# Kernel tuning notes

Measured on AMD Instinct MI355X. Metric: run time of the kernel, lower is better.

The kernel has to match this reference:

```python
import jax, jax.numpy as jnp
import numpy as np

MSK_TOK_ID = 4
SPC_TOK_IDS = (0, 1, 2, 3)
REG_W, MSK_W, SPC_W = 1.0, 1.0, 0.01
B, S, V = 8, 1024, 32000


def setup_inputs() -> dict:
    key = jax.random.key(0)
    k1, k2, k3 = jax.random.split(key, 3)
    logits_pred = jax.random.normal(k1, (B, S, V), dtype=jnp.float32)
    tokens_inp = jax.random.randint(k2, (B, S), 0, 100, dtype=jnp.int32)
    tokens_tgt = jax.random.randint(k3, (B, S), 0, V, dtype=jnp.int32)
    return {"logits_pred": logits_pred, "tokens_inp": tokens_inp, "tokens_tgt": tokens_tgt}


def _loss(logits_pred, tokens_inp, tokens_tgt):
    # torch: softmax then log(gather) == log_softmax then gather (more stable, same math)
    logp = jax.nn.log_softmax(logits_pred, axis=-1)                 # [B,S,V]
    nll = -jnp.take_along_axis(logp, tokens_tgt[..., None].astype(jnp.int32), axis=2)[..., 0]  # [B,S]

    mask_msk = tokens_inp == MSK_TOK_ID
    mask_spc = jnp.zeros_like(mask_msk)
    for t in SPC_TOK_IDS:
        mask_spc = mask_spc | (tokens_inp == t)
    mask_reg = (~mask_msk) & (~mask_spc)

    def cat_mean(mask):
        cnt = jnp.sum(mask, axis=1)                                  # [B]
        s = jnp.sum(jnp.where(mask, nll, 0.0), axis=1)               # [B]
        present = cnt > 0
        mean = jnp.where(present, s / jnp.maximum(cnt, 1).astype(nll.dtype), 0.0)
        return mean, present.astype(nll.dtype)

    m_reg, p_reg = cat_mean(mask_reg)
    m_msk, p_msk = cat_mean(mask_msk)
    m_spc, p_spc = cat_mean(mask_spc)

    num = m_reg * REG_W * p_reg + m_msk * MSK_W * p_msk + m_spc * SPC_W * p_spc
    tw = p_reg * REG_W + p_msk * MSK_W + p_spc * SPC_W              # per-item total_weight
    loss = jnp.mean(num / tw)

    def cat_avg(mean, present):
        n = jnp.sum(present)
        return jnp.where(n > 0, jnp.sum(mean) / jnp.maximum(n, 1.0), 0.0)

    return loss, cat_avg(m_reg, p_reg), cat_avg(m_msk, p_msk), cat_avg(m_spc, p_spc)


def reference(logits_pred, tokens_inp, tokens_tgt):
    # returns (loss, reg_toks_loss, msk_toks_loss, spc_toks_loss)
    return _loss(logits_pred, tokens_inp, tokens_tgt)
```

## Files before the change

### kernel.cpp

```cpp
#include <hip/hip_runtime.h>
#include <math.h>

#define NB 8
#define NS 1024
#define NV 32000

__global__ __launch_bounds__(256)
void nll_kernel(const float* __restrict__ logits,
                const int* __restrict__ tgt,
                float* __restrict__ nll) {
    const int row = blockIdx.x;
    const float* rp = logits + (size_t)row * NV;
    const int tid = threadIdx.x;

    float m = -INFINITY, s = 0.0f;
    const float4* rp4 = (const float4*)rp;
    const int n4 = NV / 4;
    for (int i = tid; i < n4; i += 256) {
        float4 x = rp4[i];
        float m4 = fmaxf(fmaxf(x.x, x.y), fmaxf(x.z, x.w));
        float nm = fmaxf(m, m4);
        s = s * __expf(m - nm)
          + __expf(x.x - nm) + __expf(x.y - nm)
          + __expf(x.z - nm) + __expf(x.w - nm);
        m = nm;
    }

    #pragma unroll
    for (int off = 1; off < 64; off <<= 1) {
        float om = __shfl_xor(m, off, 64);
        float os = __shfl_xor(s, off, 64);
        float nm = fmaxf(m, om);
        s = s * __expf(m - nm) + os * __expf(om - nm);
        m = nm;
    }

    __shared__ float sm[4], ss[4];
    const int wave = tid >> 6, lane = tid & 63;
    if (lane == 0) { sm[wave] = m; ss[wave] = s; }
    __syncthreads();
    if (tid == 0) {
        float M = sm[0], Sv = ss[0];
        #pragma unroll
        for (int w = 1; w < 4; ++w) {
            float om = sm[w], os = ss[w];
            float nm = fmaxf(M, om);
            Sv = Sv * __expf(M - nm) + os * __expf(om - nm);
            M = nm;
        }
        float lse = __logf(Sv) + M;
        float lt = rp[tgt[row]];
        nll[row] = lse - lt;
    }
}

__global__ __launch_bounds__(256)
void batch_reduce_kernel(const int* __restrict__ inp,
                         const float* __restrict__ nll,
                         float* __restrict__ part) {
    const int b = blockIdx.x;
    const int tid = threadIdx.x;
    float acc[6] = {0.f, 0.f, 0.f, 0.f, 0.f, 0.f};
    for (int i = tid; i < NS; i += 256) {
        int tok = inp[b * NS + i];
        float v = nll[b * NS + i];
        if (tok == 4)                 { acc[2] += v; acc[3] += 1.f; }
        else if ((unsigned)tok < 4u)  { acc[4] += v; acc[5] += 1.f; }
        else                          { acc[0] += v; acc[1] += 1.f; }
    }
    __shared__ float buf[6][256];
    #pragma unroll
    for (int k = 0; k < 6; ++k) buf[k][tid] = acc[k];
    __syncthreads();
    for (int off = 128; off > 0; off >>= 1) {
        if (tid < off) {
            #pragma unroll
            for (int k = 0; k < 6; ++k) buf[k][tid] += buf[k][tid + off];
        }
        __syncthreads();
    }
    if (tid == 0) {
        #pragma unroll
        for (int k = 0; k < 6; ++k) part[b * 6 + k] = buf[k][0];
    }
}

__global__ void finalize_kernel(const float* __restrict__ part,
                                float* __restrict__ out) {
    if (threadIdx.x != 0 || blockIdx.x != 0) return;
    const float W[3] = {1.0f, 1.0f, 0.01f};
    float loss_acc = 0.f;
    float sum_m[3] = {0.f, 0.f, 0.f};
    float sum_p[3] = {0.f, 0.f, 0.f};
    for (int b = 0; b < NB; ++b) {
        float num = 0.f, tw = 0.f;
        #pragma unroll
        for (int k = 0; k < 3; ++k) {
            float s = part[b * 6 + 2 * k];
            float c = part[b * 6 + 2 * k + 1];
            float p = (c > 0.f) ? 1.f : 0.f;
            float mean = (c > 0.f) ? (s / c) : 0.f;
            num += mean * W[k] * p;
            tw  += p * W[k];
            sum_m[k] += mean;
            sum_p[k] += p;
        }
        loss_acc += num / tw;
    }
    out[0] = loss_acc / (float)NB;
    #pragma unroll
    for (int k = 0; k < 3; ++k)
        out[1 + k] = (sum_p[k] > 0.f) ? (sum_m[k] / fmaxf(sum_p[k], 1.f)) : 0.f;
}

extern "C" void kernel_launch(void* const* d_in, const int* in_sizes, int n_in,
                              void* d_out, int out_size, void* d_ws, size_t ws_size,
                              hipStream_t stream) {
    const float* logits = (const float*)d_in[0];
    const int*   inp    = (const int*)d_in[1];
    const int*   tgt    = (const int*)d_in[2];
    float* out = (float*)d_out;
    float* nll  = (float*)d_ws;
    float* part = nll + NB * NS;

    nll_kernel<<<NB * NS, 256, 0, stream>>>(logits, tgt, nll);
    batch_reduce_kernel<<<NB, 256, 0, stream>>>(inp, nll, part);
    finalize_kernel<<<1, 64, 0, stream>>>(part, out);
}
```

Measured before the change: 188.7 us.

## Use unshifted exp-sum fast path for logsumexp and fuse reduce with finalize

The row kernel now sums exp(x) directly without a running max, dropping the per-element rescale exponentials. It falls back to a two-pass max-then-sum only when the sum underflows or overflows. The batch reduction and finalize kernels are merged into one 512-thread block with one wave per batch using shuffle reductions, which removes a launch. The unshifted sum can lose precision for large-magnitude logits but stays correct for well-scaled inputs.

```diff
diff --git a/kernel.cpp b/kernel.cpp
--- a/kernel.cpp
+++ b/kernel.cpp
@@ -12,105 +12,130 @@
     const int row = blockIdx.x;
     const float* rp = logits + (size_t)row * NV;
     const int tid = threadIdx.x;
-
-    float m = -INFINITY, s = 0.0f;
     const float4* rp4 = (const float4*)rp;
     const int n4 = NV / 4;
+
+    float s0 = 0.f, s1 = 0.f;
     for (int i = tid; i < n4; i += 256) {
         float4 x = rp4[i];
-        float m4 = fmaxf(fmaxf(x.x, x.y), fmaxf(x.z, x.w));
-        float nm = fmaxf(m, m4);
-        s = s * __expf(m - nm)
-          + __expf(x.x - nm) + __expf(x.y - nm)
-          + __expf(x.z - nm) + __expf(x.w - nm);
-        m = nm;
+        float e0 = __expf(x.x);
+        float e1 = __expf(x.y);
+        float e2 = __expf(x.z);
+        float e3 = __expf(x.w);
+        s0 += e0 + e1;
+        s1 += e2 + e3;
+    }
+    float s = s0 + s1;
+
+    #pragma unroll
+    for (int off = 1; off < 64; off <<= 1)
+        s += __shfl_xor(s, off, 64);
+
+    __shared__ float ssum[4];
+    __shared__ float blk_s;
+    const int wave = tid >> 6, lane = tid & 63;
+    if (lane == 0) ssum[wave] = s;
+    __syncthreads();
+    if (tid == 0) blk_s = (ssum[0] + ssum[1]) + (ssum[2] + ssum[3]);
+    __syncthreads();
+    const float S = blk_s;
+
+    if (S > 1.0e-30f && S < 3.0e38f) {
+        if (tid == 0) nll[row] = __logf(S) - rp[tgt[row]];
+        return;
     }
 
+    float m = -INFINITY;
+    for (int i = tid; i < n4; i += 256) {
+        float4 x = rp4[i];
+        m = fmaxf(m, fmaxf(fmaxf(x.x, x.y), fmaxf(x.z, x.w)));
+    }
     #pragma unroll
-    for (int off = 1; off < 64; off <<= 1) {
-        float om = __shfl_xor(m, off, 64);
-        float os = __shfl_xor(s, off, 64);
-        float nm = fmaxf(m, om);
-        s = s * __expf(m - nm) + os * __expf(om - nm);
-        m = nm;
+    for (int off = 1; off < 64; off <<= 1)
+        m = fmaxf(m, __shfl_xor(m, off, 64));
+    __shared__ float smax[4];
+    __shared__ float blk_m;
+    if (lane == 0) smax[wave] = m;
+    __syncthreads();
+    if (tid == 0)
+        blk_m = fmaxf(fmaxf(smax[0], smax[1]), fmaxf(smax[2], smax[3]));
+    __syncthreads();
+    const float M = blk_m;
+
+    float c0 = 0.f, c1 = 0.f;
+    for (int i = tid; i < n4; i += 256) {
+        float4 x = rp4[i];
+        c0 += __expf(x.x - M) + __expf(x.y - M);
+        c1 += __expf(x.z - M) + __expf(x.w - M);
     }
-
-    __shared__ float sm[4], ss[4];
-    const int wave = tid >> 6, lane = tid & 63;
-    if (lane == 0) { sm[wave] = m; ss[wave] = s; }
+    float c = c0 + c1;
+    #pragma unroll
+    for (int off = 1; off < 64; off <<= 1)
+        c += __shfl_xor(c, off, 64);
+    if (lane == 0) ssum[wave] = c;
     __syncthreads();
     if (tid == 0) {
-        float M = sm[0], Sv = ss[0];
-        #pragma unroll
-        for (int w = 1; w < 4; ++w) {
-            float om = sm[w], os = ss[w];
-            float nm = fmaxf(M, om);
-            Sv = Sv * __expf(M - nm) + os * __expf(om - nm);
-            M = nm;
-        }
-        float lse = __logf(Sv) + M;
-        float lt = rp[tgt[row]];
-        nll[row] = lse - lt;
+        float S2 = (ssum[0] + ssum[1]) + (ssum[2] + ssum[3]);
+        nll[row] = M + __logf(S2) - rp[tgt[row]];
     }
 }
 
-__global__ __launch_bounds__(256)
-void batch_reduce_kernel(const int* __restrict__ inp,
-                         const float* __restrict__ nll,
-                         float* __restrict__ part) {
-    const int b = blockIdx.x;
+__global__ __launch_bounds__(512)
+void reduce_finalize_kernel(const int* __restrict__ inp,
+                            const float* __restrict__ nll,
+                            float* __restrict__ out) {
     const int tid = threadIdx.x;
+    const int b = tid >> 6;
+    const int lane = tid & 63;
+    const int base = b * NS;
+
     float acc[6] = {0.f, 0.f, 0.f, 0.f, 0.f, 0.f};
-    for (int i = tid; i < NS; i += 256) {
-        int tok = inp[b * NS + i];
-        float v = nll[b * NS + i];
-        if (tok == 4)                 { acc[2] += v; acc[3] += 1.f; }
-        else if ((unsigned)tok < 4u)  { acc[4] += v; acc[5] += 1.f; }
-        else                          { acc[0] += v; acc[1] += 1.f; }
+    for (int i = lane; i < NS; i += 64) {
+        int tok = inp[base + i];
+        float v = nll[base + i];
+        if (tok == 4)                { acc[2] += v; acc[3] += 1.f; }
+        else if ((unsigned)tok < 4u) { acc[4] += v; acc[5] += 1.f; }
+        else                         { acc[0] += v; acc[1] += 1.f; }
     }
-    __shared__ float buf[6][256];
     #pragma unroll
-    for (int k = 0; k < 6; ++k) buf[k][tid] = acc[k];
+    for (int off = 1; off < 64; off <<= 1) {
+        #pragma unroll
+        for (int k = 0; k < 6; ++k) acc[k] += __shfl_xor(acc[k], off, 64);
+    }
+
+    __shared__ float part[NB][6];
+    if (lane == 0) {
+        #pragma unroll
+        for (int k = 0; k < 6; ++k) part[b][k] = acc[k];
+    }
     __syncthreads();
-    for (int off = 128; off > 0; off >>= 1) {
-        if (tid < off) {
+
+    if (tid == 0) {
+        const float W[3] = {1.0f, 1.0f, 0.01f};
+        float loss_acc = 0.f;
+        float sum_m[3] = {0.f, 0.f, 0.f};
+        float sum_p[3] = {0.f, 0.f, 0.f};
+        for (int bb = 0; bb < NB; ++bb) {
+            float num = 0.f, tw = 0.f;
             #pragma unroll
-            for (int k = 0; k < 6; ++k) buf[k][tid] += buf[k][tid + off];
+            for (int k = 0; k < 3; ++k) {
+                float sv = part[bb][2 * k];
+                float cn = part[bb][2 * k + 1];
+                float p = (cn > 0.f) ? 1.f : 0.f;
+                float mean = (cn > 0.f) ? (sv / cn) : 0.f;
+                num += mean * W[k] * p;
+                tw  += p * W[k];
+                sum_m[k] += mean;
+                sum_p[k] += p;
+            }
+            loss_acc += num / tw;
         }
-        __syncthreads();
+        out[0] = loss_acc / (float)NB;
+        #pragma unroll
+        for (int k = 0; k < 3; ++k)
+            out[1 + k] = (sum_p[k] > 0.f) ? (sum_m[k] / fmaxf(sum_p[k], 1.f))
+                                          : 0.f;
     }
-    if (tid == 0) {
-        #pragma unroll
-        for (int k = 0; k < 6; ++k) part[b * 6 + k] = buf[k][0];
-    }
-}
-
-__global__ void finalize_kernel(const float* __restrict__ part,
-                                float* __restrict__ out) {
-    if (threadIdx.x != 0 || blockIdx.x != 0) return;
-    const float W[3] = {1.0f, 1.0f, 0.01f};
-    float loss_acc = 0.f;
-    float sum_m[3] = {0.f, 0.f, 0.f};
-    float sum_p[3] = {0.f, 0.f, 0.f};
-    for (int b = 0; b < NB; ++b) {
-        float num = 0.f, tw = 0.f;
-        #pragma unroll
-        for (int k = 0; k < 3; ++k) {
-            float s = part[b * 6 + 2 * k];
-            float c = part[b * 6 + 2 * k + 1];
-            float p = (c > 0.f) ? 1.f : 0.f;
-            float mean = (c > 0.f) ? (s / c) : 0.f;
-            num += mean * W[k] * p;
-            tw  += p * W[k];
-            sum_m[k] += mean;
-            sum_p[k] += p;
-        }
-        loss_acc += num / tw;
-    }
-    out[0] = loss_acc / (float)NB;
-    #pragma unroll
-    for (int k = 0; k < 3; ++k)
-        out[1 + k] = (sum_p[k] > 0.f) ? (sum_m[k] / fmaxf(sum_p[k], 1.f)) : 0.f;
 }
 
 extern "C" void kernel_launch(void* const* d_in, const int* in_sizes, int n_in,
@@ -120,10 +145,8 @@
     const int*   inp    = (const int*)d_in[1];
     const int*   tgt    = (const int*)d_in[2];
     float* out = (float*)d_out;
-    float* nll  = (float*)d_ws;
-    float* part = nll + NB * NS;
+    float* nll = (float*)d_ws;
 
     nll_kernel<<<NB * NS, 256, 0, stream>>>(logits, tgt, nll);
-    batch_reduce_kernel<<<NB, 256, 0, stream>>>(inp, nll, part);
-    finalize_kernel<<<1, 64, 0, stream>>>(part, out);
+    reduce_finalize_kernel<<<1, 512, 0, stream>>>(inp, nll, out);
 }
```

Result: slower. 194.1 us (+2.8%).

## Compute logsumexp without max shift, falling back to two-pass on overflow

Applied to the files above, without the earlier changes.

Replaces the online max-rescaled softmax sum with a plain sum of exp(x), which removes the per-element max tracking and rescaling exps. It also software-pipelines the float4 loads with a fixed trip count. If the block sum underflows or overflows, it falls back to a stable two-pass max-then-sum. This relies on logits being small enough that exp does not overflow, which holds for typical inputs, and the stable path still guarantees correctness.

```diff
diff --git a/kernel.cpp b/kernel.cpp
--- a/kernel.cpp
+++ b/kernel.cpp
@@ -4,6 +4,7 @@
 #define NB 8
 #define NS 1024
 #define NV 32000
+#define N4 (NV / 4)
 
 __global__ __launch_bounds__(256)
 void nll_kernel(const float* __restrict__ logits,
@@ -11,46 +12,80 @@
                 float* __restrict__ nll) {
     const int row = blockIdx.x;
     const float* rp = logits + (size_t)row * NV;
+    const float4* rp4 = (const float4*)rp;
     const int tid = threadIdx.x;
 
-    float m = -INFINITY, s = 0.0f;
-    const float4* rp4 = (const float4*)rp;
-    const int n4 = NV / 4;
-    for (int i = tid; i < n4; i += 256) {
-        float4 x = rp4[i];
-        float m4 = fmaxf(fmaxf(x.x, x.y), fmaxf(x.z, x.w));
-        float nm = fmaxf(m, m4);
-        s = s * __expf(m - nm)
-          + __expf(x.x - nm) + __expf(x.y - nm)
-          + __expf(x.z - nm) + __expf(x.w - nm);
-        m = nm;
+    const float lt = rp[tgt[row]];
+
+    float s0 = 0.f, s1 = 0.f;
+    float4 a = rp4[tid];
+    float4 b = rp4[tid + 256];
+    int i = tid + 512;
+    for (int it = 0; it < 29; ++it, i += 256) {
+        float4 c = rp4[i];
+        s0 += __expf(a.x) + __expf(a.y);
+        s1 += __expf(a.z) + __expf(a.w);
+        a = b; b = c;
+    }
+    s0 += __expf(a.x) + __expf(a.y) + __expf(b.x) + __expf(b.y);
+    s1 += __expf(a.z) + __expf(a.w) + __expf(b.z) + __expf(b.w);
+    if (tid < 64) {
+        float4 t = rp4[31 * 256 + tid];
+        s0 += __expf(t.x) + __expf(t.y);
+        s1 += __expf(t.z) + __expf(t.w);
+    }
+    float s = s0 + s1;
+
+    #pragma unroll
+    for (int off = 1; off < 64; off <<= 1)
+        s += __shfl_xor(s, off, 64);
+
+    __shared__ float ssum[4];
+    __shared__ float blk_s;
+    const int wave = tid >> 6, lane = tid & 63;
+    if (lane == 0) ssum[wave] = s;
+    __syncthreads();
+    if (tid == 0) blk_s = (ssum[0] + ssum[1]) + (ssum[2] + ssum[3]);
+    __syncthreads();
+    const float S = blk_s;
+
+    if (S > 1.0e-30f && S < 3.0e38f) {
+        if (tid == 0) nll[row] = __logf(S) - lt;
+        return;
     }
 
+    float m = -INFINITY;
+    for (int j = tid; j < N4; j += 256) {
+        float4 x = rp4[j];
+        m = fmaxf(m, fmaxf(fmaxf(x.x, x.y), fmaxf(x.z, x.w)));
+    }
     #pragma unroll
-    for (int off = 1; off < 64; off <<= 1) {
-        float om = __shfl_xor(m, off, 64);
-        float os = __shfl_xor(s, off, 64);
-        float nm = fmaxf(m, om);
-        s = s * __expf(m - nm) + os * __expf(om - nm);
-        m = nm;
+    for (int off = 1; off < 64; off <<= 1)
+        m = fmaxf(m, __shfl_xor(m, off, 64));
+    __shared__ float smax[4];
+    __shared__ float blk_m;
+    if (lane == 0) smax[wave] = m;
+    __syncthreads();
+    if (tid == 0)
+        blk_m = fmaxf(fmaxf(smax[0], smax[1]), fmaxf(smax[2], smax[3]));
+    __syncthreads();
+    const float M = blk_m;
+
+    float c0 = 0.f, c1 = 0.f;
+    for (int j = tid; j < N4; j += 256) {
+        float4 x = rp4[j];
+        c0 += __expf(x.x - M) + __expf(x.y - M);
+        c1 += __expf(x.z - M) + __expf(x.w - M);
     }
-
-    __shared__ float sm[4], ss[4];
-    const int wave = tid >> 6, lane = tid & 63;
-    if (lane == 0) { sm[wave] = m; ss[wave] = s; }
+    float c = c0 + c1;
+    #pragma unroll
+    for (int off = 1; off < 64; off <<= 1)
+        c += __shfl_xor(c, off, 64);
+    if (lane == 0) ssum[wave] = c;
     __syncthreads();
     if (tid == 0) {
-        float M = sm[0], Sv = ss[0];
-        #pragma unroll
-        for (int w = 1; w < 4; ++w) {
-            float om = sm[w], os = ss[w];
-            float nm = fmaxf(M, om);
-            Sv = Sv * __expf(M - nm) + os * __expf(om - nm);
-            M = nm;
-        }
-        float lse = __logf(Sv) + M;
-        float lt = rp[tgt[row]];
-        nll[row] = lse - lt;
+        float S2 = (ssum[0] + ssum[1]) + (ssum[2] + ssum[3]);
+        nll[row] = M + __logf(S2) - lt;
     }
 }
 
```

After: 182.7 us (median of 2 runs). 3.2% less time.
